# Kernel optimization log

Hardware: AMD Instinct MI355X
Metric: run time of the kernel (lower is better)

Reference implementation:

```python
import jax, jax.numpy as jnp
import numpy as np

N_HEAD = 16
N_KV_HEAD = 4
N_EMBD = 2048
HEAD_DIM = N_EMBD // N_HEAD
RMS_EPS = float(np.finfo(np.float32).eps)  # torch F.rms_norm default eps


def setup_inputs() -> dict:
    key = jax.random.key(0)
    ks = jax.random.split(key, 7)
    B, T = 2, 2048
    s = 0.02
    return {
        "x": jax.random.normal(ks[0], (B, T, N_EMBD), jnp.float32),
        "cos": jax.random.uniform(ks[1], (T, 1, HEAD_DIM), jnp.float32),
        "sin": jax.random.uniform(ks[2], (T, 1, HEAD_DIM), jnp.float32),
        "wq": jax.random.normal(ks[3], (N_HEAD * HEAD_DIM, N_EMBD), jnp.float32) * s,
        "wk": jax.random.normal(ks[4], (N_KV_HEAD * HEAD_DIM, N_EMBD), jnp.float32) * s,
        "wv": jax.random.normal(ks[5], (N_KV_HEAD * HEAD_DIM, N_EMBD), jnp.float32) * s,
        "wproj": jax.random.normal(ks[6], (N_EMBD, N_EMBD), jnp.float32) * s,
    }


def _rotate_half(x):
    h = x.shape[-1] // 2
    return jnp.concatenate([-x[..., h:], x[..., :h]], axis=-1)


def _apply_rope(x, cos, sin):  # x: [B, T, H, D]; cos/sin: [T, 1, D]
    return x * cos + _rotate_half(x) * sin


def _rms_norm(x):
    var = jnp.mean(jnp.square(x), axis=-1, keepdims=True)
    return x * jax.lax.rsqrt(var + RMS_EPS)


def reference(x, cos, sin, wq, wk, wv, wproj):
    B, T, C = x.shape
    group = N_HEAD // N_KV_HEAD
    q = (x @ wq.T).reshape(B, T, N_HEAD, HEAD_DIM)
    k = (x @ wk.T).reshape(B, T, N_KV_HEAD, HEAD_DIM)
    v = (x @ wv.T).reshape(B, T, N_KV_HEAD, HEAD_DIM)
    q = _rms_norm(_apply_rope(q, cos, sin))  # RoPE then QK RMSNorm
    k = _rms_norm(_apply_rope(k, cos, sin))
    # to [B, H, T, D]; expand kv heads for GQA
    q = q.transpose(0, 2, 1, 3)
    k = jnp.repeat(k.transpose(0, 2, 1, 3), group, axis=1)
    v = jnp.repeat(v.transpose(0, 2, 1, 3), group, axis=1)
    scale = 1.0 / jnp.sqrt(jnp.asarray(HEAD_DIM, x.dtype))
    scores = jnp.einsum('bhqd,bhkd->bhqk', q, k) * scale
    causal = jnp.tril(jnp.ones((T, T), bool))
    scores = jnp.where(causal, scores, jnp.asarray(-jnp.inf, scores.dtype))
    attn = jax.nn.softmax(scores, axis=-1)
    y = jnp.einsum('bhqk,bhkd->bhqd', attn, v)
    y = y.transpose(0, 2, 1, 3).reshape(B, T, C)
    return y @ wproj.T
```

## Files before the change

### kernel.cpp

```cpp
#include <hip/hip_runtime.h>
#include <hip/hip_bf16.h>

typedef __hip_bfloat16 bf16;
typedef __attribute__((ext_vector_type(8))) __bf16 bf16x8;
typedef __attribute__((ext_vector_type(4))) float f32x4;

#define MFMA16(a, b, c) __builtin_amdgcn_mfma_f32_16x16x32_bf16((a), (b), (c), 0, 0, 0)

#define BT 4096
#define CE 2048
#define NQKV 3072
#define TSEQ 2048
#define HD 128

#define QSCALE (0.08838834764831845f * 1.4426950408889634f)
#define M2 16.3222f

__device__ __forceinline__ void gld16(const void* g, void* l)
{
    __builtin_amdgcn_global_load_lds(
        (const __attribute__((address_space(1))) void*)g,
        (__attribute__((address_space(3))) void*)l, 16, 0, 0);
}

__global__ void detect_dtype(const unsigned short* __restrict__ x, int* __restrict__ flag)
{
    __shared__ int cnt;
    if (threadIdx.x == 0) cnt = 0;
    __syncthreads();
    unsigned short w = x[2 * threadIdx.x];
    int e = (w >> 7) & 0xFF;
    atomicAdd(&cnt, (e >= 117 && e <= 130) ? 1 : 0);
    __syncthreads();
    if (threadIdx.x == 0) *flag = (cnt < 128) ? 1 : 0;
}

__device__ __forceinline__ void stage8(short* dst, const void* src, size_t eoff, bool f32)
{
    if (f32) {
        const float* s = (const float*)src + eoff;
        float4 f0 = *(const float4*)s;
        float4 f1 = *(const float4*)(s + 4);
        bf16x8 v;
        v[0] = (__bf16)f0.x; v[1] = (__bf16)f0.y; v[2] = (__bf16)f0.z; v[3] = (__bf16)f0.w;
        v[4] = (__bf16)f1.x; v[5] = (__bf16)f1.y; v[6] = (__bf16)f1.z; v[7] = (__bf16)f1.w;
        *(bf16x8*)dst = v;
    } else {
        *(uint4*)dst = *(const uint4*)((const bf16*)src + eoff);
    }
}

__device__ __forceinline__ float ldf(const void* p, int i, bool f32)
{
    return f32 ? ((const float*)p)[i] : __bfloat162float(((const bf16*)p)[i]);
}

__global__ __launch_bounds__(256)
void conv_bf16(const void* __restrict__ src, bf16* __restrict__ dst,
               const int* __restrict__ flagp)
{
    const bool f = *flagp != 0;
    size_t i8 = (size_t)blockIdx.x * 256 + threadIdx.x;
    stage8((short*)(dst + i8 * 8), src, i8 * 8, f);
}

__global__ __launch_bounds__(256)
void gemm_bt(const void* __restrict__ A, const bf16* __restrict__ W,
             void* __restrict__ C, int M, int N, int K, int lda,
             int aGate, int oGate, const int* __restrict__ flagp)
{
    __shared__ short As[128][32];
    __shared__ short Bs[128][32];

    const int f = *flagp;
    const bool aF = aGate && f, oF = oGate && f;

    const int tid   = threadIdx.x;
    const int lane  = tid & 63;
    const int wid   = tid >> 6;
    const int row16 = lane & 15;
    const int quad  = lane >> 4;
    const int wr    = wid >> 1;
    const int wc    = wid & 1;
    const int m0    = blockIdx.y * 128;
    const int n0    = blockIdx.x * 128;

    const int rl4 = wid * 16 + (lane >> 2);
    const int c8  = (lane & 3) * 8;

    f32x4 acc[4][4];
#pragma unroll
    for (int i = 0; i < 4; i++)
#pragma unroll
        for (int j = 0; j < 4; j++)
            acc[i][j] = (f32x4){0.f, 0.f, 0.f, 0.f};

    for (int k0 = 0; k0 < K; k0 += 32) {
#pragma unroll
        for (int i = 0; i < 2; i++) {
            int r = i * 64 + rl4;
            gld16(W + (size_t)(n0 + r) * K + k0 + c8, &Bs[r][c8]);
        }
        if (!aF) {
#pragma unroll
            for (int i = 0; i < 2; i++) {
                int r = i * 64 + rl4;
                gld16((const bf16*)A + (size_t)(m0 + r) * lda + k0 + c8, &As[r][c8]);
            }
        } else {
#pragma unroll
            for (int i = 0; i < 2; i++) {
                int c = i * 256 + tid;
                int row = c >> 2, col = (c & 3) << 3;
                stage8(&As[row][col], A, (size_t)(m0 + row) * lda + k0 + col, true);
            }
        }
        __syncthreads();

        bf16x8 af[4], bfv[4];
#pragma unroll
        for (int mi = 0; mi < 4; mi++)
            af[mi] = *(const bf16x8*)&As[wr * 64 + mi * 16 + row16][quad * 8];
#pragma unroll
        for (int ni = 0; ni < 4; ni++)
            bfv[ni] = *(const bf16x8*)&Bs[wc * 64 + ni * 16 + row16][quad * 8];
#pragma unroll
        for (int mi = 0; mi < 4; mi++)
#pragma unroll
            for (int ni = 0; ni < 4; ni++)
                acc[mi][ni] = MFMA16(af[mi], bfv[ni], acc[mi][ni]);
        __syncthreads();
    }

#pragma unroll
    for (int mi = 0; mi < 4; mi++) {
        int rowb = m0 + wr * 64 + mi * 16 + quad * 4;
#pragma unroll
        for (int ni = 0; ni < 4; ni++) {
            int col = n0 + wc * 64 + ni * 16 + row16;
#pragma unroll
            for (int r = 0; r < 4; r++) {
                size_t idx = (size_t)(rowb + r) * N + col;
                float  v   = acc[mi][ni][r];
                if (oF) ((float*)C)[idx] = v;
                else    ((bf16*)C)[idx]  = __float2bfloat16(v);
            }
        }
    }
}

template<int MI, int NIW>
__global__ __launch_bounds__(512, 2)
void gemmP(const bf16* __restrict__ A, const bf16* __restrict__ W,
           void* __restrict__ C, int M, int N, int K, int lda,
           int oGate, const int* __restrict__ flagp)
{
    constexpr int BM     = MI * 32;
    constexpr int BN     = NIW * 64;
    constexpr int ABYTES = BM * 128;
    constexpr int BBYTES = BN * 128;
    constexpr int AUL    = BM / 64;
    constexpr int BUL    = BN / 64;

    __shared__ __bf16 As[2][BM][64];
    __shared__ __bf16 Bs[2][BN][64];

    const bool oF = oGate && (*flagp != 0);

    const int gx  = gridDim.x;
    const int lin = blockIdx.y * gx + blockIdx.x;
    const int cpx = (gx * gridDim.y) >> 3;
    const int swzid = (lin & 7) * cpx + (lin >> 3);
    const int bx = swzid % gx;
    const int by = swzid / gx;

    const int tid   = threadIdx.x;
    const int lane  = tid & 63;
    const int wid   = tid >> 6;
    const int row16 = lane & 15;
    const int quad  = lane >> 4;
    const int wr    = wid >> 2;
    const int wc    = wid & 3;
    const int m0    = by * BM;
    const int n0    = bx * BN;
    const int NT    = K >> 6;

    const int srow = tid >> 3;
    const int sc8  = ((tid & 7) ^ (srow & 7)) * 8;
    const bf16* Ag = A + (size_t)(m0 + srow) * lda + sc8;
    const bf16* Bg = W + (size_t)(n0 + srow) * K   + sc8;
    char* const AsB = (char*)As;
    char* const BsB = (char*)Bs;
    const int sdst = tid * 16;

    auto stA = [&](int kt, int b) {
#pragma unroll
        for (int u = 0; u < AUL; ++u)
            gld16(Ag + (size_t)(u * 64) * lda + kt * 64,
                  AsB + b * ABYTES + u * 8192 + sdst);
    };
    auto stB = [&](int kt, int b) {
#pragma unroll
        for (int u = 0; u < BUL; ++u)
            gld16(Bg + (size_t)(u * 64) * K + kt * 64,
                  BsB + b * BBYTES + u * 8192 + sdst);
    };

    const int swz  = ((quad ^ (row16 & 7)) * 16);
    const int swz1 = (((4 + quad) ^ (row16 & 7)) * 16);
    const int aRow = wr * (MI * 16) + row16;
    const int bRow = wc * (NIW * 16) + row16;

    auto ldA = [&](int b, int mi, int kk) -> bf16x8 {
        return *(const bf16x8*)(AsB + b * ABYTES + (aRow + mi * 16) * 128
                                + (kk ? swz1 : swz));
    };
    auto ldB = [&](int b, int ni, int kk) -> bf16x8 {
        return *(const bf16x8*)(BsB + b * BBYTES + (bRow + ni * 16) * 128
                                + (kk ? swz1 : swz));
    };

    f32x4 acc[MI][NIW];
#pragma unroll
    for (int i = 0; i < MI; i++)
#pragma unroll
        for (int j = 0; j < NIW; j++)
            acc[i][j] = (f32x4){0.f, 0.f, 0.f, 0.f};

    stA(0, 0); stB(0, 0);
    asm volatile("s_waitcnt vmcnt(0)" ::: "memory");
    __builtin_amdgcn_s_barrier();
    __builtin_amdgcn_sched_barrier(0);

    for (int t = 0; t < NT; ++t) {
        const int rb = t & 1;
        const int wb = rb ^ 1;

        bf16x8 bfr[NIW][2];
#pragma unroll
        for (int ni = 0; ni < NIW; ni++)
#pragma unroll
            for (int kk = 0; kk < 2; kk++)
                bfr[ni][kk] = ldB(rb, ni, kk);
        bf16x8 a0[2][2];
#pragma unroll
        for (int i = 0; i < 2; i++)
#pragma unroll
            for (int kk = 0; kk < 2; kk++)
                a0[i][kk] = ldA(rb, i, kk);

        if (t + 1 < NT) { stB(t + 1, wb); stA(t + 1, wb); }

        __builtin_amdgcn_s_setprio(1);
#pragma unroll
        for (int kk = 0; kk < 2; kk++)
#pragma unroll
            for (int i = 0; i < 2; i++)
#pragma unroll
                for (int ni = 0; ni < NIW; ni++)
                    acc[i][ni] = MFMA16(a0[i][kk], bfr[ni][kk], acc[i][ni]);
        __builtin_amdgcn_s_setprio(0);

#pragma unroll
        for (int p = 1; p < MI / 2; ++p) {
            bf16x8 ap[2][2];
#pragma unroll
            for (int i = 0; i < 2; i++)
#pragma unroll
                for (int kk = 0; kk < 2; kk++)
                    ap[i][kk] = ldA(rb, 2 * p + i, kk);
            __builtin_amdgcn_s_setprio(1);
#pragma unroll
            for (int kk = 0; kk < 2; kk++)
#pragma unroll
                for (int i = 0; i < 2; i++)
#pragma unroll
                    for (int ni = 0; ni < NIW; ni++)
                        acc[2 * p + i][ni] =
                            MFMA16(ap[i][kk], bfr[ni][kk], acc[2 * p + i][ni]);
            __builtin_amdgcn_s_setprio(0);
        }

        asm volatile("s_waitcnt vmcnt(0)" ::: "memory");
        __builtin_amdgcn_s_barrier();
        __builtin_amdgcn_sched_barrier(0);
    }

#pragma unroll
    for (int mi = 0; mi < MI; mi++) {
        int rowb = m0 + wr * (MI * 16) + mi * 16 + quad * 4;
#pragma unroll
        for (int ni = 0; ni < NIW; ni++) {
            int col = n0 + wc * (NIW * 16) + ni * 16 + row16;
#pragma unroll
            for (int r = 0; r < 4; r++) {
                size_t idx = (size_t)(rowb + r) * N + col;
                float  v   = acc[mi][ni][r];
                if (oF) ((float*)C)[idx] = v;
                else    ((bf16*)C)[idx]  = __float2bfloat16(v);
            }
        }
    }
}

__global__ __launch_bounds__(256)
void rope_rms(bf16* __restrict__ qkv, const void* __restrict__ cosp,
              const void* __restrict__ sinp, const int* __restrict__ flagp)
{
    const bool f = *flagp != 0;
    const int wg   = blockIdx.x * 4 + (threadIdx.x >> 6);
    const int lane = threadIdx.x & 63;
    const int s    = wg % 20;
    const int m    = wg / 20;
    const int t    = m & (TSEQ - 1);

    const int col = (s < 16) ? s * HD : CE + (s - 16) * HD;
    bf16* p = qkv + (size_t)m * NQKV + col;

    float xlo = __bfloat162float(p[lane]);
    float xhi = __bfloat162float(p[lane + 64]);
    float cl  = ldf(cosp, t * HD + lane, f);
    float sl  = ldf(sinp, t * HD + lane, f);
    float ch  = ldf(cosp, t * HD + 64 + lane, f);
    float sh  = ldf(sinp, t * HD + 64 + lane, f);

    float rlo = xlo * cl - xhi * sl;
    float rhi = xhi * ch + xlo * sh;

    float ss = rlo * rlo + rhi * rhi;
#pragma unroll
    for (int off = 32; off > 0; off >>= 1)
        ss += __shfl_xor(ss, off, 64);
    float inv = rsqrtf(ss * (1.0f / 128.0f) + 1.1920929e-07f);
    if (s < 16) inv *= QSCALE;

    p[lane]      = __float2bfloat16(rlo * inv);
    p[lane + 64] = __float2bfloat16(rhi * inv);
}

__global__ __launch_bounds__(256)
void vtrans(const bf16* __restrict__ qkv, bf16* __restrict__ vt)
{
    __shared__ __bf16 tl[64][136];

    const int tid = threadIdx.x;
    const int bh  = blockIdx.x >> 5;
    const int t0  = (blockIdx.x & 31) * 64;
    const int b   = bh >> 2;
    const int hk  = bh & 3;

    const bf16* src = qkv + ((size_t)(b * TSEQ + t0)) * NQKV + 2560 + hk * HD;
#pragma unroll
    for (int it = 0; it < 4; ++it) {
        int idx  = it * 256 + tid;
        int trow = idx >> 4;
        int dcol = (idx & 15) * 8;
        *(uint4*)&tl[trow][dcol] = *(const uint4*)(src + (size_t)trow * NQKV + dcol);
    }
    __syncthreads();

    bf16* dst = vt + ((size_t)(bh * HD)) * TSEQ + t0;
#pragma unroll
    for (int it = 0; it < 4; ++it) {
        int idx  = it * 256 + tid;
        int drow = idx >> 3;
        int tcol = (idx & 7) * 8;
        bf16x8 v;
#pragma unroll
        for (int j = 0; j < 8; ++j)
            v[j] = tl[tcol + j][drow];
        *(bf16x8*)(dst + (size_t)drow * TSEQ + tcol) = v;
    }
}

__global__ __launch_bounds__(512, 2)
void attn(bf16* __restrict__ qkv, const bf16* __restrict__ vt)
{
    __shared__ char lds[81920];
    char* const KsB = lds;
    char* const VsB = lds + 32768;
    char* const PlB = lds + 65536;

    const int tid   = threadIdx.x;
    const int lane  = tid & 63;
    const int wid   = tid >> 6;
    const int row16 = lane & 15;
    const int quad  = lane >> 4;
    const int b   = blockIdx.y >> 2;
    const int hk  = blockIdx.y & 3;
    const int hp  = wid & 1;
    const int mh  = (wid >> 1) & 1;
    const int ks  = wid >> 2;
    const int h0  = hk * 4 + hp * 2;
    const int p   = blockIdx.x;

    const bf16* Kp = qkv + ((size_t)(b * TSEQ)) * NQKV + CE + hk * HD;
    const bf16* Vp = vt + ((size_t)(b * 4 + hk) * HD) * TSEQ;

    auto stage = [&](int buf, int k0) {
#pragma unroll
        for (int i = 0; i < 2; i++) {
            int kr = (wid << 3) + i * 4 + (lane >> 4);
            int kc = (lane & 15) ^ (kr & 7);
            gld16(Kp + (size_t)(k0 + kr) * NQKV + kc * 8,
                  KsB + buf * 16384 + ((wid << 3) + i * 4) * 256 + lane * 16);
            int vr = (wid << 4) + i * 8 + (lane >> 3);
            int vc = (lane & 7) ^ (vr & 7);
            gld16(Vp + (size_t)vr * TSEQ + k0 + vc * 8,
                  VsB + buf * 16384 + ((wid << 4) + i * 8) * 128 + lane * 16);
        }
    };

    for (int pass = 0; pass < 2; ++pass) {
        const int xi  = pass ? 63 - p : p;
        const int nkt = (xi >> 1) + 1;
        const int qr0 = xi * 32 + mh * 16;

        const bf16* Q = qkv + ((size_t)(b * TSEQ + qr0)) * NQKV + h0 * HD;
        bf16x8 aq[2][4];
#pragma unroll
        for (int h2 = 0; h2 < 2; h2++)
#pragma unroll
            for (int ds = 0; ds < 4; ds++)
                aq[h2][ds] = *(const bf16x8*)(Q + h2 * HD
                             + (size_t)row16 * NQKV + ds * 32 + quad * 8);

        f32x4 o[2][8];
#pragma unroll
        for (int h2 = 0; h2 < 2; h2++)
#pragma unroll
            for (int dt = 0; dt < 8; dt++)
                o[h2][dt] = (f32x4){0.f, 0.f, 0.f, 0.f};
        f32x4 lsum[2] = {(f32x4){0.f,0.f,0.f,0.f}, (f32x4){0.f,0.f,0.f,0.f}};

        __syncthreads();
        stage(0, 0);
        __syncthreads();

        for (int t = 0; t < nkt; ++t) {
            const int cur = t & 1;
            if (t + 1 < nkt) stage(cur ^ 1, (t + 1) * 64);

            f32x4 s[2][2];
#pragma unroll
            for (int h2 = 0; h2 < 2; h2++)
#pragma unroll
                for (int kgl = 0; kgl < 2; kgl++)
                    s[h2][kgl] = (f32x4){0.f, 0.f, 0.f, 0.f};
            __builtin_amdgcn_s_setprio(1);
#pragma unroll
            for (int ds = 0; ds < 4; ds++) {
#pragma unroll
                for (int kgl = 0; kgl < 2; kgl++) {
                    int krow = (ks * 2 + kgl) * 16 + row16;
                    int phys = (ds * 4 + quad) ^ (krow & 7);
                    bf16x8 kf = *(const bf16x8*)(KsB + cur * 16384
                                                 + krow * 256 + phys * 16);
                    s[0][kgl] = MFMA16(aq[0][ds], kf, s[0][kgl]);
                    s[1][kgl] = MFMA16(aq[1][ds], kf, s[1][kgl]);
                }
            }
            __builtin_amdgcn_s_setprio(0);

            const bool diag = (t == nkt - 1);
            const int  kbase = t * 64 + ks * 32;
            const int  r16h = row16 >> 3;
            const int  r16l = (row16 & 7) * 2;
#pragma unroll
            for (int h2 = 0; h2 < 2; h2++) {
#pragma unroll
                for (int r = 0; r < 4; r++) {
                    int prow = quad * 4 + r;
                    int qrow = qr0 + prow;
                    float pv0, pv1;
                    {
                        float e0 = __builtin_amdgcn_exp2f(s[h2][0][r] - M2);
                        float e1 = __builtin_amdgcn_exp2f(s[h2][1][r] - M2);
                        pv0 = (!diag || (kbase + row16      <= qrow)) ? e0 : 0.f;
                        pv1 = (!diag || (kbase + 16 + row16 <= qrow)) ? e1 : 0.f;
                    }
                    lsum[h2][r] += pv0 + pv1;
                    char* base = PlB + wid * 2048 + h2 * 1024 + prow * 64;
                    *(__bf16*)(base + (((0 * 2 + r16h) ^ (prow & 3)) << 4) + r16l)
                        = (__bf16)pv0;
                    *(__bf16*)(base + (((1 * 2 + r16h) ^ (prow & 3)) << 4) + r16l)
                        = (__bf16)pv1;
                }
            }
            __asm__ volatile("" ::: "memory");

            __builtin_amdgcn_s_setprio(1);
            bf16x8 pf0 = *(const bf16x8*)(PlB + wid * 2048 + row16 * 64
                                          + ((quad ^ (row16 & 3)) << 4));
            bf16x8 pf1 = *(const bf16x8*)(PlB + wid * 2048 + 1024 + row16 * 64
                                          + ((quad ^ (row16 & 3)) << 4));
#pragma unroll
            for (int dt = 0; dt < 8; dt++) {
                int vrow = dt * 16 + row16;
                int phys = (ks * 4 + quad) ^ (vrow & 7);
                bf16x8 vf = *(const bf16x8*)(VsB + cur * 16384
                                             + vrow * 128 + phys * 16);
                o[0][dt] = MFMA16(pf0, vf, o[0][dt]);
                o[1][dt] = MFMA16(pf1, vf, o[1][dt]);
            }
            __builtin_amdgcn_s_setprio(0);
            __asm__ volatile("" ::: "memory");
            __syncthreads();
        }

        const int g = (hp << 1) | mh;
        char* const scr = lds + g * 16384;
        __syncthreads();
        if (ks) {
#pragma unroll
            for (int h2 = 0; h2 < 2; h2++)
#pragma unroll
                for (int dt = 0; dt < 8; dt++)
                    *(f32x4*)(scr + (h2 * 8 + dt) * 1024 + lane * 16) = o[h2][dt];
            *(f32x4*)(PlB + g * 4096 + lane * 32)      = lsum[0];
            *(f32x4*)(PlB + g * 4096 + lane * 32 + 16) = lsum[1];
        }
        __syncthreads();
        if (!ks) {
#pragma unroll
            for (int h2 = 0; h2 < 2; h2++)
#pragma unroll
                for (int dt = 0; dt < 8; dt++)
                    o[h2][dt] += *(const f32x4*)(scr + (h2 * 8 + dt) * 1024
                                                 + lane * 16);
            f32x4 l0 = *(const f32x4*)(PlB + g * 4096 + lane * 32);
            f32x4 l1 = *(const f32x4*)(PlB + g * 4096 + lane * 32 + 16);
#pragma unroll
            for (int h2 = 0; h2 < 2; h2++) {
#pragma unroll
                for (int r = 0; r < 4; r++) {
                    float l = lsum[h2][r] + (h2 ? l1[r] : l0[r]);
#pragma unroll
                    for (int off = 1; off < 16; off <<= 1)
                        l += __shfl_xor(l, off, 64);
                    float rl = 1.0f / l;
                    int trow = qr0 + quad * 4 + r;
                    bf16* dst = qkv + ((size_t)(b * TSEQ + trow)) * NQKV
                                + (h0 + h2) * HD;
#pragma unroll
                    for (int dt = 0; dt < 8; dt++)
                        dst[dt * 16 + row16] = __float2bfloat16(o[h2][dt][r] * rl);
                }
            }
        }
    }
}

extern "C" void kernel_launch(void* const* d_in, const int* in_sizes, int n_in,
                              void* d_out, int out_size, void* d_ws, size_t ws_size,
                              hipStream_t stream)
{
    bf16* qkv   = (bf16*)d_ws;
    bf16* vt    = qkv + (size_t)BT * NQKV;
    bf16* wqkvb = vt + (size_t)2 * 4 * HD * TSEQ;
    int* flagp  = (int*)(wqkvb + (size_t)NQKV * CE);
    bf16* xb    = wqkvb + (size_t)NQKV * CE + 16;

    const size_t need = ((size_t)BT * NQKV + (size_t)2 * 4 * HD * TSEQ
                         + (size_t)NQKV * CE + 16 + (size_t)BT * CE) * sizeof(bf16);
    const bool useXb = ws_size >= need;

    detect_dtype<<<1, 256, 0, stream>>>((const unsigned short*)d_in[0], flagp);

    conv_bf16<<<(2048 * 2048 / 8) / 256, 256, 0, stream>>>(d_in[3], wqkvb, flagp);
    conv_bf16<<<(512 * 2048 / 8) / 256, 256, 0, stream>>>(d_in[4], wqkvb + (size_t)2048 * 2048, flagp);
    conv_bf16<<<(512 * 2048 / 8) / 256, 256, 0, stream>>>(d_in[5], wqkvb + (size_t)2560 * 2048, flagp);

    if (useXb) {
        conv_bf16<<<(BT * CE / 8) / 256, 256, 0, stream>>>(d_in[0], xb, flagp);
        gemmP<8, 3><<<dim3(NQKV / 192, BT / 256), 512, 0, stream>>>(
            xb, wqkvb, qkv, BT, NQKV, CE, CE, 0, flagp);
    } else {
        gemm_bt<<<dim3(NQKV / 128, BT / 128), 256, 0, stream>>>(
            d_in[0], wqkvb, qkv, BT, NQKV, CE, CE, 1, 0, flagp);
    }

    conv_bf16<<<(2048 * 2048 / 8) / 256, 256, 0, stream>>>(d_in[6], wqkvb, flagp);

    vtrans<<<256, 256, 0, stream>>>(qkv, vt);

    rope_rms<<<(BT * 20) / 4, 256, 0, stream>>>(qkv, d_in[1], d_in[2], flagp);

    attn<<<dim3(32, 2 * 4), 512, 0, stream>>>(qkv, vt);

    if (useXb) {
        gemmP<4, 4><<<dim3(CE / 256, BT / 128), 512, 0, stream>>>(
            qkv, wqkvb, d_out, BT, CE, CE, NQKV, 1, flagp);
    } else {
        gemm_bt<<<dim3(CE / 128, BT / 128), 256, 0, stream>>>(
            qkv, wqkvb, d_out, BT, CE, CE, NQKV, 0, 1, flagp);
    }
}
```

Before: 304.2 us.

## Triple-buffer GEMM B tiles and merge conversion and rope/vtrans launches

```diff
diff --git a/kernel.cpp b/kernel.cpp
--- a/kernel.cpp
+++ b/kernel.cpp
@@ -65,6 +65,25 @@
 }
 
 __global__ __launch_bounds__(256)
+void conv_all(const void* __restrict__ wq, const void* __restrict__ wk,
+              const void* __restrict__ wv, const void* __restrict__ x,
+              bf16* __restrict__ wqkvb, bf16* __restrict__ xb,
+              const int* __restrict__ flagp)
+{
+    const bool f = *flagp != 0;
+    size_t i8 = (size_t)blockIdx.x * 256 + threadIdx.x;
+    if (i8 < 524288) {
+        stage8((short*)(wqkvb + i8 * 8), wq, i8 * 8, f);
+    } else if (i8 < 655360) {
+        stage8((short*)(wqkvb + i8 * 8), wk, (i8 - 524288) * 8, f);
+    } else if (i8 < 786432) {
+        stage8((short*)(wqkvb + i8 * 8), wv, (i8 - 655360) * 8, f);
+    } else {
+        stage8((short*)(xb + (i8 - 786432) * 8), x, (i8 - 786432) * 8, f);
+    }
+}
+
+__global__ __launch_bounds__(256)
 void gemm_bt(const void* __restrict__ A, const bf16* __restrict__ W,
              void* __restrict__ C, int M, int N, int K, int lda,
              int aGate, int oGate, const int* __restrict__ flagp)
@@ -151,7 +170,7 @@
 
 template<int MI, int NIW>
 __global__ __launch_bounds__(512, 2)
-void gemmP(const bf16* __restrict__ A, const bf16* __restrict__ W,
+void gemmS(const bf16* __restrict__ A, const bf16* __restrict__ W,
            void* __restrict__ C, int M, int N, int K, int lda,
            int oGate, const int* __restrict__ flagp)
 {
@@ -163,7 +182,7 @@
     constexpr int BUL    = BN / 64;
 
     __shared__ __bf16 As[2][BM][64];
-    __shared__ __bf16 Bs[2][BN][64];
+    __shared__ __bf16 Bs[3][BN][64];
 
     const bool oF = oGate && (*flagp != 0);
 
@@ -193,17 +212,17 @@
     char* const BsB = (char*)Bs;
     const int sdst = tid * 16;
 
-    auto stA = [&](int kt, int b) {
+    auto stA = [&](int kt, int s) {
 #pragma unroll
         for (int u = 0; u < AUL; ++u)
             gld16(Ag + (size_t)(u * 64) * lda + kt * 64,
-                  AsB + b * ABYTES + u * 8192 + sdst);
+                  AsB + s * ABYTES + u * 8192 + sdst);
     };
-    auto stB = [&](int kt, int b) {
+    auto stB = [&](int kt, int s) {
 #pragma unroll
         for (int u = 0; u < BUL; ++u)
             gld16(Bg + (size_t)(u * 64) * K + kt * 64,
-                  BsB + b * BBYTES + u * 8192 + sdst);
+                  BsB + s * BBYTES + u * 8192 + sdst);
     };
 
     const int swz  = ((quad ^ (row16 & 7)) * 16);
@@ -211,12 +230,12 @@
     const int aRow = wr * (MI * 16) + row16;
     const int bRow = wc * (NIW * 16) + row16;
 
-    auto ldA = [&](int b, int mi, int kk) -> bf16x8 {
-        return *(const bf16x8*)(AsB + b * ABYTES + (aRow + mi * 16) * 128
+    auto ldA = [&](int sb, int mi, int kk) -> bf16x8 {
+        return *(const bf16x8*)(AsB + sb + (aRow + mi * 16) * 128
                                 + (kk ? swz1 : swz));
     };
-    auto ldB = [&](int b, int ni, int kk) -> bf16x8 {
-        return *(const bf16x8*)(BsB + b * BBYTES + (bRow + ni * 16) * 128
+    auto ldB = [&](int sb, int ni, int kk) -> bf16x8 {
+        return *(const bf16x8*)(BsB + sb + (bRow + ni * 16) * 128
                                 + (kk ? swz1 : swz));
     };
 
@@ -227,29 +246,31 @@
         for (int j = 0; j < NIW; j++)
             acc[i][j] = (f32x4){0.f, 0.f, 0.f, 0.f};
 
-    stA(0, 0); stB(0, 0);
-    asm volatile("s_waitcnt vmcnt(0)" ::: "memory");
+    stA(0, 0); stB(0, 0); stB(1, 1);
+    if constexpr (BUL == 3) asm volatile("s_waitcnt vmcnt(3)" ::: "memory");
+    else                    asm volatile("s_waitcnt vmcnt(4)" ::: "memory");
     __builtin_amdgcn_s_barrier();
     __builtin_amdgcn_sched_barrier(0);
 
     for (int t = 0; t < NT; ++t) {
-        const int rb = t & 1;
-        const int wb = rb ^ 1;
+        const int sbA = (t & 1) * ABYTES;
+        const int sbB = (t % 3) * BBYTES;
 
         bf16x8 bfr[NIW][2];
 #pragma unroll
         for (int ni = 0; ni < NIW; ni++)
 #pragma unroll
             for (int kk = 0; kk < 2; kk++)
-                bfr[ni][kk] = ldB(rb, ni, kk);
+                bfr[ni][kk] = ldB(sbB, ni, kk);
         bf16x8 a0[2][2];
 #pragma unroll
         for (int i = 0; i < 2; i++)
 #pragma unroll
             for (int kk = 0; kk < 2; kk++)
-                a0[i][kk] = ldA(rb, i, kk);
-
-        if (t + 1 < NT) { stB(t + 1, wb); stA(t + 1, wb); }
+                a0[i][kk] = ldA(sbA, i, kk);
+
+        if (t + 1 < NT) stA(t + 1, (t + 1) & 1);
+        if (t + 2 < NT) stB(t + 2, (t + 2) % 3);
 
         __builtin_amdgcn_s_setprio(1);
 #pragma unroll
@@ -268,7 +289,7 @@
             for (int i = 0; i < 2; i++)
 #pragma unroll
                 for (int kk = 0; kk < 2; kk++)
-                    ap[i][kk] = ldA(rb, 2 * p + i, kk);
+                    ap[i][kk] = ldA(sbA, 2 * p + i, kk);
             __builtin_amdgcn_s_setprio(1);
 #pragma unroll
             for (int kk = 0; kk < 2; kk++)
@@ -281,7 +302,12 @@
             __builtin_amdgcn_s_setprio(0);
         }
 
-        asm volatile("s_waitcnt vmcnt(0)" ::: "memory");
+        if (t + 2 < NT) {
+            if constexpr (BUL == 3) asm volatile("s_waitcnt vmcnt(3)" ::: "memory");
+            else                    asm volatile("s_waitcnt vmcnt(4)" ::: "memory");
+        } else {
+            asm volatile("s_waitcnt vmcnt(0)" ::: "memory");
+        }
         __builtin_amdgcn_s_barrier();
         __builtin_amdgcn_sched_barrier(0);
     }
@@ -304,72 +330,72 @@
 }
 
 __global__ __launch_bounds__(256)
-void rope_rms(bf16* __restrict__ qkv, const void* __restrict__ cosp,
-              const void* __restrict__ sinp, const int* __restrict__ flagp)
-{
-    const bool f = *flagp != 0;
-    const int wg   = blockIdx.x * 4 + (threadIdx.x >> 6);
-    const int lane = threadIdx.x & 63;
-    const int s    = wg % 20;
-    const int m    = wg / 20;
-    const int t    = m & (TSEQ - 1);
-
-    const int col = (s < 16) ? s * HD : CE + (s - 16) * HD;
-    bf16* p = qkv + (size_t)m * NQKV + col;
-
-    float xlo = __bfloat162float(p[lane]);
-    float xhi = __bfloat162float(p[lane + 64]);
-    float cl  = ldf(cosp, t * HD + lane, f);
-    float sl  = ldf(sinp, t * HD + lane, f);
-    float ch  = ldf(cosp, t * HD + 64 + lane, f);
-    float sh  = ldf(sinp, t * HD + 64 + lane, f);
-
-    float rlo = xlo * cl - xhi * sl;
-    float rhi = xhi * ch + xlo * sh;
-
-    float ss = rlo * rlo + rhi * rhi;
-#pragma unroll
-    for (int off = 32; off > 0; off >>= 1)
-        ss += __shfl_xor(ss, off, 64);
-    float inv = rsqrtf(ss * (1.0f / 128.0f) + 1.1920929e-07f);
-    if (s < 16) inv *= QSCALE;
-
-    p[lane]      = __float2bfloat16(rlo * inv);
-    p[lane + 64] = __float2bfloat16(rhi * inv);
-}
-
-__global__ __launch_bounds__(256)
-void vtrans(const bf16* __restrict__ qkv, bf16* __restrict__ vt)
+void vtrans_rope(bf16* __restrict__ qkv, bf16* __restrict__ vt,
+                 const void* __restrict__ cosp, const void* __restrict__ sinp,
+                 const int* __restrict__ flagp)
 {
     __shared__ __bf16 tl[64][136];
-
     const int tid = threadIdx.x;
-    const int bh  = blockIdx.x >> 5;
-    const int t0  = (blockIdx.x & 31) * 64;
-    const int b   = bh >> 2;
-    const int hk  = bh & 3;
-
-    const bf16* src = qkv + ((size_t)(b * TSEQ + t0)) * NQKV + 2560 + hk * HD;
-#pragma unroll
-    for (int it = 0; it < 4; ++it) {
-        int idx  = it * 256 + tid;
-        int trow = idx >> 4;
-        int dcol = (idx & 15) * 8;
-        *(uint4*)&tl[trow][dcol] = *(const uint4*)(src + (size_t)trow * NQKV + dcol);
-    }
-    __syncthreads();
-
-    bf16* dst = vt + ((size_t)(bh * HD)) * TSEQ + t0;
-#pragma unroll
-    for (int it = 0; it < 4; ++it) {
-        int idx  = it * 256 + tid;
-        int drow = idx >> 3;
-        int tcol = (idx & 7) * 8;
-        bf16x8 v;
-#pragma unroll
-        for (int j = 0; j < 8; ++j)
-            v[j] = tl[tcol + j][drow];
-        *(bf16x8*)(dst + (size_t)drow * TSEQ + tcol) = v;
+
+    if (blockIdx.x < 20480) {
+        const bool f = *flagp != 0;
+        const int wg   = blockIdx.x * 4 + (tid >> 6);
+        const int lane = tid & 63;
+        const int s    = wg % 20;
+        const int m    = wg / 20;
+        const int t    = m & (TSEQ - 1);
+
+        const int col = (s < 16) ? s * HD : CE + (s - 16) * HD;
+        bf16* p = qkv + (size_t)m * NQKV + col;
+
+        float xlo = __bfloat162float(p[lane]);
+        float xhi = __bfloat162float(p[lane + 64]);
+        float cl  = ldf(cosp, t * HD + lane, f);
+        float sl  = ldf(sinp, t * HD + lane, f);
+        float ch  = ldf(cosp, t * HD + 64 + lane, f);
+        float sh  = ldf(sinp, t * HD + 64 + lane, f);
+
+        float rlo = xlo * cl - xhi * sl;
+        float rhi = xhi * ch + xlo * sh;
+
+        float ss = rlo * rlo + rhi * rhi;
+#pragma unroll
+        for (int off = 32; off > 0; off >>= 1)
+            ss += __shfl_xor(ss, off, 64);
+        float inv = rsqrtf(ss * (1.0f / 128.0f) + 1.1920929e-07f);
+        if (s < 16) inv *= QSCALE;
+
+        p[lane]      = __float2bfloat16(rlo * inv);
+        p[lane + 64] = __float2bfloat16(rhi * inv);
+    } else {
+        const int bi  = blockIdx.x - 20480;
+        const int bh  = bi >> 5;
+        const int t0  = (bi & 31) * 64;
+        const int b   = bh >> 2;
+        const int hk  = bh & 3;
+
+        const bf16* src = qkv + ((size_t)(b * TSEQ + t0)) * NQKV + 2560 + hk * HD;
+#pragma unroll
+        for (int it = 0; it < 4; ++it) {
+            int idx  = it * 256 + tid;
+            int trow = idx >> 4;
+            int dcol = (idx & 15) * 8;
+            *(uint4*)&tl[trow][dcol] = *(const uint4*)(src + (size_t)trow * NQKV + dcol);
+        }
+        __syncthreads();
+
+        bf16* dst = vt + ((size_t)(bh * HD)) * TSEQ + t0;
+#pragma unroll
+        for (int it = 0; it < 4; ++it) {
+            int idx  = it * 256 + tid;
+            int drow = idx >> 3;
+            int tcol = (idx & 7) * 8;
+            bf16x8 v;
+#pragma unroll
+            for (int j = 0; j < 8; ++j)
+                v[j] = tl[tcol + j][drow];
+            *(bf16x8*)(dst + (size_t)drow * TSEQ + tcol) = v;
+        }
     }
 }
 
@@ -567,13 +593,11 @@
 
     detect_dtype<<<1, 256, 0, stream>>>((const unsigned short*)d_in[0], flagp);
 
-    conv_bf16<<<(2048 * 2048 / 8) / 256, 256, 0, stream>>>(d_in[3], wqkvb, flagp);
-    conv_bf16<<<(512 * 2048 / 8) / 256, 256, 0, stream>>>(d_in[4], wqkvb + (size_t)2048 * 2048, flagp);
-    conv_bf16<<<(512 * 2048 / 8) / 256, 256, 0, stream>>>(d_in[5], wqkvb + (size_t)2560 * 2048, flagp);
+    conv_all<<<useXb ? 7168 : 3072, 256, 0, stream>>>(
+        d_in[3], d_in[4], d_in[5], d_in[0], wqkvb, xb, flagp);
 
     if (useXb) {
-        conv_bf16<<<(BT * CE / 8) / 256, 256, 0, stream>>>(d_in[0], xb, flagp);
-        gemmP<8, 3><<<dim3(NQKV / 192, BT / 256), 512, 0, stream>>>(
+        gemmS<8, 3><<<dim3(NQKV / 192, BT / 256), 512, 0, stream>>>(
             xb, wqkvb, qkv, BT, NQKV, CE, CE, 0, flagp);
     } else {
         gemm_bt<<<dim3(NQKV / 128, BT / 128), 256, 0, stream>>>(
@@ -582,14 +606,12 @@
 
     conv_bf16<<<(2048 * 2048 / 8) / 256, 256, 0, stream>>>(d_in[6], wqkvb, flagp);
 
-    vtrans<<<256, 256, 0, stream>>>(qkv, vt);
-
-    rope_rms<<<(BT * 20) / 4, 256, 0, stream>>>(qkv, d_in[1], d_in[2], flagp);
+    vtrans_rope<<<20736, 256, 0, stream>>>(qkv, vt, d_in[1], d_in[2], flagp);
 
     attn<<<dim3(32, 2 * 4), 512, 0, stream>>>(qkv, vt);
 
     if (useXb) {
-        gemmP<4, 4><<<dim3(CE / 256, BT / 128), 512, 0, stream>>>(
+        gemmS<4, 4><<<dim3(CE / 256, BT / 128), 512, 0, stream>>>(
             qkv, wqkvb, d_out, BT, CE, CE, NQKV, 1, flagp);
     } else {
         gemm_bt<<<dim3(CE / 128, BT / 128), 256, 0, stream>>>(
```

Result: no change. 298.9 us (-1.7%).
